# Kernel tuning notes

Measured on AMD Instinct MI355X. Metric: run time of the kernel, lower is better.

## Reference

```python
import jax, jax.numpy as jnp
import numpy as np
import math

D = 1024
H = 16
S = 2048

def setup_inputs() -> dict:
    key = jax.random.key(0)
    k1, k2, k3 = jax.random.split(key, 3)
    x = jax.random.normal(k1, (2, S, D), dtype=jnp.float32)
    # nn.Linear(D, 3D): weight [3D, D], bias [3D]
    W = jax.random.normal(k2, (3 * D, D), dtype=jnp.float32) / math.sqrt(D)
    b = jax.random.normal(k3, (3 * D,), dtype=jnp.float32) * 0.01
    return {"x": x, "W": W, "b": b}

def reference(x, W, b):
    N, C, Dm = x.shape
    hd = Dm // H
    z = jnp.einsum('ncd,ed->nce', x, W) + b  # [N, C, 3D]
    k = z[:, :, :Dm].reshape(N, C, H, hd).transpose(0, 2, 1, 3)
    q = z[:, :, Dm:2 * Dm].reshape(N, C, H, hd).transpose(0, 2, 1, 3)
    v = z[:, :, 2 * Dm:].reshape(N, C, H, hd).transpose(0, 2, 1, 3)
    # NOTE: original scales by 1/sqrt(D) (full dim), not 1/sqrt(head_dim)
    scores = jnp.einsum('nhqd,nhkd->nhqk', q, k) / math.sqrt(Dm)
    causal = jnp.tril(jnp.ones((C, C), dtype=bool))
    scores = jnp.where(causal[None, None], scores, -jnp.inf)
    attn = jax.nn.softmax(scores, axis=-1)
    out = jnp.einsum('nhqk,nhkd->nhqd', attn, v)
    return out.transpose(0, 2, 1, 3).reshape(N, C, Dm)
```

## Files before the change

kernel.cpp:

```cpp
#include <hip/hip_runtime.h>
#include <hip/hip_bf16.h>

#define D_MODEL 1024
#define NH 16
#define HD 64
#define S_LEN 2048
#define NB 2
#define M_TOT 4096
#define N3 3072

typedef __attribute__((ext_vector_type(8))) short bf16x8;
typedef __attribute__((ext_vector_type(4))) float f32x4;
typedef __attribute__((ext_vector_type(4))) unsigned short u16x4;

__device__ __forceinline__ unsigned short f2bf(float f) {
    unsigned int u = __float_as_uint(f);
    u += 0x7fffu + ((u >> 16) & 1u);
    return (unsigned short)(u >> 16);
}

#define GLOAD_LDS(gp, lp)                                                      \
    __builtin_amdgcn_global_load_lds(                                          \
        (const __attribute__((address_space(1))) void*)(gp),                   \
        (__attribute__((address_space(3))) void*)(lp), 16, 0, 0)

__global__ __launch_bounds__(256) void cast_f32_bf16(
    const float* __restrict__ in, unsigned short* __restrict__ out, int n4) {
    int i = blockIdx.x * 256 + threadIdx.x;
    if (i < n4) {
        float4 v = reinterpret_cast<const float4*>(in)[i];
        u16x4 o;
        o.x = f2bf(v.x); o.y = f2bf(v.y); o.z = f2bf(v.z); o.w = f2bf(v.w);
        reinterpret_cast<u16x4*>(out)[i] = o;
    }
}

#define BM 128
#define BN 128
#define BK 64

__global__ __launch_bounds__(256) void qkv_gemm(
    const unsigned short* __restrict__ A, const unsigned short* __restrict__ B,
    const float* __restrict__ bias, unsigned short* __restrict__ Z) {
    __shared__ unsigned short As[BM * BK];
    __shared__ unsigned short Bs[BN * BK];

    const int t = threadIdx.x;
    const int lane = t & 63;
    const int wid = t >> 6;
    const int wr = wid >> 1, wc = wid & 1;
    const int bm = blockIdx.y, bn = blockIdx.x;
    const int lr = lane & 15;
    const int lg = lane >> 4;
    const int srow = lane >> 3;
    const int sslot = lane & 7;

    f32x4 acc[4][4] = {};

    for (int k0 = 0; k0 < 1024; k0 += BK) {
        __syncthreads();
#pragma unroll
        for (int p = 0; p < 4; ++p) {
            int rb = wid * 32 + p * 8;
            int row = rb + srow;
            int seg = sslot ^ (row & 7);
            GLOAD_LDS(&A[(size_t)(bm * BM + row) * 1024 + k0 + seg * 8],
                      &As[rb * BK]);
            GLOAD_LDS(&B[(size_t)(bn * BN + row) * 1024 + k0 + seg * 8],
                      &Bs[rb * BK]);
        }
        __syncthreads();
#pragma unroll
        for (int ks = 0; ks < 2; ++ks) {
            bf16x8 af[4], bfr[4];
#pragma unroll
            for (int m = 0; m < 4; ++m) {
                int row = wr * 64 + m * 16 + lr;
                int slot = (ks * 4 + lg) ^ (row & 7);
                af[m] = *reinterpret_cast<const bf16x8*>(&As[row * BK + slot * 8]);
            }
#pragma unroll
            for (int n = 0; n < 4; ++n) {
                int row = wc * 64 + n * 16 + lr;
                int slot = (ks * 4 + lg) ^ (row & 7);
                bfr[n] = *reinterpret_cast<const bf16x8*>(&Bs[row * BK + slot * 8]);
            }
#pragma unroll
            for (int m = 0; m < 4; ++m)
#pragma unroll
                for (int n = 0; n < 4; ++n)
                    acc[m][n] = __builtin_amdgcn_mfma_f32_16x16x32_bf16(
                        af[m], bfr[n], acc[m][n], 0, 0, 0);
        }
    }
#pragma unroll
    for (int m = 0; m < 4; ++m) {
        int row = bm * BM + wr * 64 + m * 16 + lg * 4;
#pragma unroll
        for (int n = 0; n < 4; ++n) {
            int col = bn * BN + wc * 64 + n * 16 + lr;
            float bv = bias[col];
#pragma unroll
            for (int i = 0; i < 4; ++i) {
                Z[(size_t)(row + i) * N3 + col] = f2bf(acc[m][n][i] + bv);
            }
        }
    }
}

__global__ __launch_bounds__(256) void transpose_v(
    const unsigned short* __restrict__ Z, unsigned short* __restrict__ Vt) {
    __shared__ unsigned short tile[64][72];
    int bid = blockIdx.x;
    int nh = bid >> 5;
    int cb = bid & 31;
    int n = nh >> 4, h = nh & 15;
    int t = threadIdx.x;
#pragma unroll
    for (int p = 0; p < 4; ++p) {
        int idx = p * 256 + t;
        int r = idx >> 4;
        int cg = idx & 15;
        u16x4 v = *reinterpret_cast<const u16x4*>(
            &Z[(size_t)(n * S_LEN + cb * 64 + r) * N3 + 2 * D_MODEL + h * HD + cg * 4]);
        *reinterpret_cast<u16x4*>(&tile[r][cg * 4]) = v;
    }
    __syncthreads();
#pragma unroll
    for (int p = 0; p < 4; ++p) {
        int idx = p * 256 + t;
        int d = idx >> 4;
        int cg = idx & 15;
        u16x4 o;
        o.x = tile[cg * 4 + 0][d];
        o.y = tile[cg * 4 + 1][d];
        o.z = tile[cg * 4 + 2][d];
        o.w = tile[cg * 4 + 3][d];
        *reinterpret_cast<u16x4*>(
            &Vt[((size_t)nh * 64 + d) * S_LEN + cb * 64 + cg * 4]) = o;
    }
}

__global__ __launch_bounds__(256) void attn(
    const unsigned short* __restrict__ Z, const unsigned short* __restrict__ Vt,
    float* __restrict__ Out) {
    const int ilin = blockIdx.y * 32 + blockIdx.x;
    const int head32 = (ilin & 7) * 4 + ((ilin >> 3) & 3);
    const int qb = 31 - (ilin >> 5);
    const int n = head32 >> 4, h = head32 & 15;

    __shared__ unsigned short Kt[2][64 * 64];
    __shared__ unsigned short Vs[2][64 * 64];
    __shared__ unsigned short p_lds[4][16][72];

    const int t = threadIdx.x;
    const int lane = t & 63, w = t >> 6;
    const int lr = lane & 15, lg = lane >> 4;
    const int srow = lane >> 3, sslot = lane & 7;

    const size_t zrowQ = (size_t)(n * S_LEN + qb * 64 + w * 16 + lr) * N3 + D_MODEL + h * HD;
    bf16x8 qf[2];
    qf[0] = *reinterpret_cast<const bf16x8*>(&Z[zrowQ + lg * 8]);
    qf[1] = *reinterpret_cast<const bf16x8*>(&Z[zrowQ + 32 + lg * 8]);

    auto STAGE = [&](int buf, int kb) {
#pragma unroll
        for (int p = 0; p < 2; ++p) {
            int rb = w * 16 + p * 8;
            int row = rb + srow;
            int seg = sslot ^ (row & 7);
            GLOAD_LDS(&Z[(size_t)(n * S_LEN + kb * 64 + row) * N3 + h * HD + seg * 8],
                      &Kt[buf][rb * 64]);
            GLOAD_LDS(&Vt[((size_t)head32 * 64 + row) * S_LEN + kb * 64 + seg * 8],
                      &Vs[buf][rb * 64]);
        }
    };

    f32x4 o[4] = {};
    float mrun[4], lrun[4];
#pragma unroll
    for (int i = 0; i < 4; ++i) { mrun[i] = -1e30f; lrun[i] = 0.f; }

    const int qrow_base = qb * 64 + w * 16 + lg * 4;

    STAGE(0, 0);
    int cur = 0;
    for (int kb = 0; kb <= qb; ++kb) {
        __syncthreads();
        if (kb < qb) STAGE(cur ^ 1, kb + 1);
        const unsigned short* Kc = &Kt[cur][0];
        const unsigned short* Vc = &Vs[cur][0];

        f32x4 s[4];
#pragma unroll
        for (int cf = 0; cf < 4; ++cf) {
            int row = cf * 16 + lr;
            bf16x8 kf0 = *reinterpret_cast<const bf16x8*>(
                &Kc[row * 64 + ((lg) ^ (row & 7)) * 8]);
            bf16x8 kf1 = *reinterpret_cast<const bf16x8*>(
                &Kc[row * 64 + ((lg + 4) ^ (row & 7)) * 8]);
            f32x4 a = {};
            a = __builtin_amdgcn_mfma_f32_16x16x32_bf16(qf[0], kf0, a, 0, 0, 0);
            a = __builtin_amdgcn_mfma_f32_16x16x32_bf16(qf[1], kf1, a, 0, 0, 0);
            s[cf] = a;
        }
        const bool diag = (kb == qb);
#pragma unroll
        for (int cf = 0; cf < 4; ++cf) {
            int kcol = kb * 64 + cf * 16 + lr;
#pragma unroll
            for (int i = 0; i < 4; ++i) {
                float v = s[cf][i] * 0.03125f;
                if (diag && kcol > qrow_base + i) v = -1e30f;
                s[cf][i] = v;
            }
        }
#pragma unroll
        for (int i = 0; i < 4; ++i) {
            float v = fmaxf(fmaxf(s[0][i], s[1][i]), fmaxf(s[2][i], s[3][i]));
            v = fmaxf(v, __shfl_xor(v, 1));
            v = fmaxf(v, __shfl_xor(v, 2));
            v = fmaxf(v, __shfl_xor(v, 4));
            v = fmaxf(v, __shfl_xor(v, 8));
            float mn = fmaxf(mrun[i], v);
            float corr = __expf(mrun[i] - mn);
            mrun[i] = mn;
            float sum = 0.f;
#pragma unroll
            for (int cf = 0; cf < 4; ++cf) {
                float p = __expf(s[cf][i] - mn);
                s[cf][i] = p;
                sum += p;
            }
            sum += __shfl_xor(sum, 1);
            sum += __shfl_xor(sum, 2);
            sum += __shfl_xor(sum, 4);
            sum += __shfl_xor(sum, 8);
            lrun[i] = lrun[i] * corr + sum;
#pragma unroll
            for (int cfd = 0; cfd < 4; ++cfd) o[cfd][i] *= corr;
        }
#pragma unroll
        for (int cf = 0; cf < 4; ++cf)
#pragma unroll
            for (int i = 0; i < 4; ++i)
                p_lds[w][lg * 4 + i][cf * 16 + lr] = f2bf(s[cf][i]);
#pragma unroll
        for (int ks = 0; ks < 2; ++ks) {
            bf16x8 pf = *reinterpret_cast<const bf16x8*>(&p_lds[w][lr][ks * 32 + lg * 8]);
#pragma unroll
            for (int cfd = 0; cfd < 4; ++cfd) {
                int vrow = cfd * 16 + lr;
                bf16x8 vf = *reinterpret_cast<const bf16x8*>(
                    &Vc[vrow * 64 + ((ks * 4 + lg) ^ (vrow & 7)) * 8]);
                o[cfd] = __builtin_amdgcn_mfma_f32_16x16x32_bf16(pf, vf, o[cfd], 0, 0, 0);
            }
        }
        cur ^= 1;
    }
#pragma unroll
    for (int cfd = 0; cfd < 4; ++cfd) {
        int d = h * HD + cfd * 16 + lr;
#pragma unroll
        for (int i = 0; i < 4; ++i) {
            int q = qb * 64 + w * 16 + lg * 4 + i;
            Out[(size_t)(n * S_LEN + q) * D_MODEL + d] = o[cfd][i] / lrun[i];
        }
    }
}

extern "C" void kernel_launch(void* const* d_in, const int* in_sizes, int n_in,
                              void* d_out, int out_size, void* d_ws, size_t ws_size,
                              hipStream_t stream) {
    const float* x = (const float*)d_in[0];
    const float* W = (const float*)d_in[1];
    const float* b = (const float*)d_in[2];
    float* out = (float*)d_out;

    char* ws = (char*)d_ws;
    unsigned short* xb = (unsigned short*)ws;
    unsigned short* Wb = (unsigned short*)(ws + (size_t)8 * 1024 * 1024);
    unsigned short* Z  = (unsigned short*)(ws + (size_t)14 * 1024 * 1024);
    unsigned short* Vt = (unsigned short*)(ws + (size_t)38 * 1024 * 1024);

    cast_f32_bf16<<<4096, 256, 0, stream>>>(x, xb, M_TOT * D_MODEL / 4);
    cast_f32_bf16<<<3072, 256, 0, stream>>>(W, Wb, N3 * D_MODEL / 4);
    qkv_gemm<<<dim3(N3 / BN, M_TOT / BM), 256, 0, stream>>>(xb, Wb, b, Z);
    transpose_v<<<1024, 256, 0, stream>>>(Z, Vt);
    attn<<<dim3(S_LEN / 64, NB * NH), 256, 0, stream>>>(Z, Vt, out);
}
```

Measured before the change: 189.1 us.

## Transpose score MFMA, prescale Q with log2e, lazy softmax rescale, merge cast kernels

Folds the 1/32 scale and log2(e) into Q once so the softmax can use exp2 without a per-element multiply. Swaps the MFMA operand order so each lane holds one query row, which removes the per-row shuffle reductions and lets P be written to LDS as packed 32-bit stores. Adds a lazy rescale that only updates the running max when it grows by more than 8 (in log2 units), plus s_setprio hints around the MFMA blocks. The two cast launches become one kernel. Rounding Q to bf16 after scaling adds a small precision risk.

```diff
diff --git a/kernel.cpp b/kernel.cpp
--- a/kernel.cpp
+++ b/kernel.cpp
@@ -18,21 +18,30 @@
     u += 0x7fffu + ((u >> 16) & 1u);
     return (unsigned short)(u >> 16);
 }
+__device__ __forceinline__ float bf2f(unsigned short s) {
+    return __uint_as_float((unsigned int)s << 16);
+}
 
 #define GLOAD_LDS(gp, lp)                                                      \
     __builtin_amdgcn_global_load_lds(                                          \
         (const __attribute__((address_space(1))) void*)(gp),                   \
         (__attribute__((address_space(3))) void*)(lp), 16, 0, 0)
 
-__global__ __launch_bounds__(256) void cast_f32_bf16(
-    const float* __restrict__ in, unsigned short* __restrict__ out, int n4) {
+__global__ __launch_bounds__(256) void cast_both(
+    const float* __restrict__ x, const float* __restrict__ W,
+    unsigned short* __restrict__ xb, unsigned short* __restrict__ Wb) {
+    const int nx = M_TOT * D_MODEL / 4;
+    const int nw = N3 * D_MODEL / 4;
     int i = blockIdx.x * 256 + threadIdx.x;
-    if (i < n4) {
-        float4 v = reinterpret_cast<const float4*>(in)[i];
-        u16x4 o;
-        o.x = f2bf(v.x); o.y = f2bf(v.y); o.z = f2bf(v.z); o.w = f2bf(v.w);
-        reinterpret_cast<u16x4*>(out)[i] = o;
-    }
+    const float* src;
+    unsigned short* dst;
+    int j;
+    if (i < nx) { src = x; dst = xb; j = i; }
+    else { j = i - nx; if (j >= nw) return; src = W; dst = Wb; }
+    float4 v = reinterpret_cast<const float4*>(src)[j];
+    u16x4 o;
+    o.x = f2bf(v.x); o.y = f2bf(v.y); o.z = f2bf(v.z); o.w = f2bf(v.w);
+    reinterpret_cast<u16x4*>(dst)[j] = o;
 }
 
 #define BM 128
@@ -158,10 +167,19 @@
     const int lr = lane & 15, lg = lane >> 4;
     const int srow = lane >> 3, sslot = lane & 7;
 
+    const float SCL = 0.03125f * 1.44269504f;
+
     const size_t zrowQ = (size_t)(n * S_LEN + qb * 64 + w * 16 + lr) * N3 + D_MODEL + h * HD;
     bf16x8 qf[2];
-    qf[0] = *reinterpret_cast<const bf16x8*>(&Z[zrowQ + lg * 8]);
-    qf[1] = *reinterpret_cast<const bf16x8*>(&Z[zrowQ + 32 + lg * 8]);
+#pragma unroll
+    for (int f = 0; f < 2; ++f) {
+        bf16x8 raw = *reinterpret_cast<const bf16x8*>(&Z[zrowQ + f * 32 + lg * 8]);
+        bf16x8 sc;
+#pragma unroll
+        for (int j = 0; j < 8; ++j)
+            sc[j] = (short)f2bf(bf2f((unsigned short)raw[j]) * SCL);
+        qf[f] = sc;
+    }
 
     auto STAGE = [&](int buf, int kb) {
 #pragma unroll
@@ -177,11 +195,7 @@
     };
 
     f32x4 o[4] = {};
-    float mrun[4], lrun[4];
-#pragma unroll
-    for (int i = 0; i < 4; ++i) { mrun[i] = -1e30f; lrun[i] = 0.f; }
-
-    const int qrow_base = qb * 64 + w * 16 + lg * 4;
+    float mrun = -1e30f, lrun = 0.f;
 
     STAGE(0, 0);
     int cur = 0;
@@ -192,6 +206,7 @@
         const unsigned short* Vc = &Vs[cur][0];
 
         f32x4 s[4];
+        __builtin_amdgcn_s_setprio(1);
 #pragma unroll
         for (int cf = 0; cf < 4; ++cf) {
             int row = cf * 16 + lr;
@@ -200,51 +215,68 @@
             bf16x8 kf1 = *reinterpret_cast<const bf16x8*>(
                 &Kc[row * 64 + ((lg + 4) ^ (row & 7)) * 8]);
             f32x4 a = {};
-            a = __builtin_amdgcn_mfma_f32_16x16x32_bf16(qf[0], kf0, a, 0, 0, 0);
-            a = __builtin_amdgcn_mfma_f32_16x16x32_bf16(qf[1], kf1, a, 0, 0, 0);
+            a = __builtin_amdgcn_mfma_f32_16x16x32_bf16(kf0, qf[0], a, 0, 0, 0);
+            a = __builtin_amdgcn_mfma_f32_16x16x32_bf16(kf1, qf[1], a, 0, 0, 0);
             s[cf] = a;
         }
-        const bool diag = (kb == qb);
+        __builtin_amdgcn_s_setprio(0);
+
+        if (kb == qb) {
+            const int qloc = w * 16 + lr;
+#pragma unroll
+            for (int cf = 0; cf < 4; ++cf) {
+                int kbase = cf * 16 + lg * 4;
+#pragma unroll
+                for (int i = 0; i < 4; ++i)
+                    if (kbase + i > qloc) s[cf][i] = -1e30f;
+            }
+        }
+
+        float pm;
+        {
+            f32x4 m4 = s[0];
+#pragma unroll
+            for (int cf = 1; cf < 4; ++cf) {
+                m4[0] = fmaxf(m4[0], s[cf][0]); m4[1] = fmaxf(m4[1], s[cf][1]);
+                m4[2] = fmaxf(m4[2], s[cf][2]); m4[3] = fmaxf(m4[3], s[cf][3]);
+            }
+            pm = fmaxf(fmaxf(m4[0], m4[1]), fmaxf(m4[2], m4[3]));
+            pm = fmaxf(pm, __shfl_xor(pm, 16));
+            pm = fmaxf(pm, __shfl_xor(pm, 32));
+        }
+        if (!__all(pm - mrun <= 8.0f)) {
+            float mn = fmaxf(mrun, pm);
+            float corr = exp2f(mrun - mn);
+            mrun = mn;
+            lrun *= corr;
+#pragma unroll
+            for (int i = 0; i < 4; ++i) {
+                float ci = __shfl(corr, lg * 4 + i);
+#pragma unroll
+                for (int cfd = 0; cfd < 4; ++cfd) o[cfd][i] *= ci;
+            }
+        }
+        float sum = 0.f;
 #pragma unroll
         for (int cf = 0; cf < 4; ++cf) {
-            int kcol = kb * 64 + cf * 16 + lr;
 #pragma unroll
             for (int i = 0; i < 4; ++i) {
-                float v = s[cf][i] * 0.03125f;
-                if (diag && kcol > qrow_base + i) v = -1e30f;
-                s[cf][i] = v;
-            }
-        }
-#pragma unroll
-        for (int i = 0; i < 4; ++i) {
-            float v = fmaxf(fmaxf(s[0][i], s[1][i]), fmaxf(s[2][i], s[3][i]));
-            v = fmaxf(v, __shfl_xor(v, 1));
-            v = fmaxf(v, __shfl_xor(v, 2));
-            v = fmaxf(v, __shfl_xor(v, 4));
-            v = fmaxf(v, __shfl_xor(v, 8));
-            float mn = fmaxf(mrun[i], v);
-            float corr = __expf(mrun[i] - mn);
-            mrun[i] = mn;
-            float sum = 0.f;
-#pragma unroll
-            for (int cf = 0; cf < 4; ++cf) {
-                float p = __expf(s[cf][i] - mn);
+                float p = exp2f(s[cf][i] - mrun);
                 s[cf][i] = p;
                 sum += p;
             }
-            sum += __shfl_xor(sum, 1);
-            sum += __shfl_xor(sum, 2);
-            sum += __shfl_xor(sum, 4);
-            sum += __shfl_xor(sum, 8);
-            lrun[i] = lrun[i] * corr + sum;
-#pragma unroll
-            for (int cfd = 0; cfd < 4; ++cfd) o[cfd][i] *= corr;
-        }
-#pragma unroll
-        for (int cf = 0; cf < 4; ++cf)
-#pragma unroll
-            for (int i = 0; i < 4; ++i)
-                p_lds[w][lg * 4 + i][cf * 16 + lr] = f2bf(s[cf][i]);
+            unsigned int lo01 = (unsigned int)f2bf(s[cf][0]) |
+                                ((unsigned int)f2bf(s[cf][1]) << 16);
+            unsigned int lo23 = (unsigned int)f2bf(s[cf][2]) |
+                                ((unsigned int)f2bf(s[cf][3]) << 16);
+            *reinterpret_cast<unsigned int*>(&p_lds[w][lr][cf * 16 + lg * 4]) = lo01;
+            *reinterpret_cast<unsigned int*>(&p_lds[w][lr][cf * 16 + lg * 4 + 2]) = lo23;
+        }
+        sum += __shfl_xor(sum, 16);
+        sum += __shfl_xor(sum, 32);
+        lrun += sum;
+
+        __builtin_amdgcn_s_setprio(1);
 #pragma unroll
         for (int ks = 0; ks < 2; ++ks) {
             bf16x8 pf = *reinterpret_cast<const bf16x8*>(&p_lds[w][lr][ks * 32 + lg * 8]);
@@ -256,15 +288,18 @@
                 o[cfd] = __builtin_amdgcn_mfma_f32_16x16x32_bf16(pf, vf, o[cfd], 0, 0, 0);
             }
         }
+        __builtin_amdgcn_s_setprio(0);
         cur ^= 1;
     }
 #pragma unroll
-    for (int cfd = 0; cfd < 4; ++cfd) {
-        int d = h * HD + cfd * 16 + lr;
-#pragma unroll
-        for (int i = 0; i < 4; ++i) {
-            int q = qb * 64 + w * 16 + lg * 4 + i;
-            Out[(size_t)(n * S_LEN + q) * D_MODEL + d] = o[cfd][i] / lrun[i];
+    for (int i = 0; i < 4; ++i) {
+        float li = __shfl(lrun, lg * 4 + i);
+        float inv = 1.0f / li;
+        int q = qb * 64 + w * 16 + lg * 4 + i;
+#pragma unroll
+        for (int cfd = 0; cfd < 4; ++cfd) {
+            int d = h * HD + cfd * 16 + lr;
+            Out[(size_t)(n * S_LEN + q) * D_MODEL + d] = o[cfd][i] * inv;
         }
     }
 }
@@ -283,9 +318,8 @@
     unsigned short* Z  = (unsigned short*)(ws + (size_t)14 * 1024 * 1024);
     unsigned short* Vt = (unsigned short*)(ws + (size_t)38 * 1024 * 1024);
 
-    cast_f32_bf16<<<4096, 256, 0, stream>>>(x, xb, M_TOT * D_MODEL / 4);
-    cast_f32_bf16<<<3072, 256, 0, stream>>>(W, Wb, N3 * D_MODEL / 4);
+    cast_both<<<7168, 256, 0, stream>>>(x, W, xb, Wb);
     qkv_gemm<<<dim3(N3 / BN, M_TOT / BM), 256, 0, stream>>>(xb, Wb, b, Z);
     transpose_v<<<1024, 256, 0, stream>>>(Z, Vt);
-    attn<<<dim3(S_LEN / 64, NB * NH), 256, 0, stream>>>(Z, Vt, out);
-}
+    attn<<<dim3(32, 32), 256, 0, stream>>>(Z, Vt, out);
+}
```

Result: faster. 173.3 us (-8.4%).
